# Kernel tuning notes

Hardware: AMD Instinct MI355X
Metric: run time of the kernel (lower is better)

Reference implementation:

```python
import jax, jax.numpy as jnp
import numpy as np

EPS = 1e-5

def yat_dense(x, kernel, bias, alpha):
    # scaled by (sqrt(F)/log(1+F))**alpha, plus bias.
    y = x @ kernel  # [..., F]
    dist = jnp.sum(x * x, axis=-1, keepdims=True) + jnp.sum(kernel * kernel, axis=0) - 2.0 * y
    out = (y * y) / (dist + EPS)
    F = kernel.shape[1]
    scale = (jnp.sqrt(jnp.float32(F)) / jnp.log1p(jnp.float32(F))) ** alpha
    return out * scale + bias

def setup_inputs() -> dict:
    key = jax.random.key(0)
    ks = jax.random.split(key, 8)
    B, T, C = 8, 1024, 1024
    x = jax.random.normal(ks[0], (B, T, C), dtype=jnp.float32)
    mask = jnp.tril(jnp.ones((T, T), dtype=bool))[None, None, :, :]  # causal [1,1,T,T]
    W_attn = jax.random.normal(ks[1], (C, 3 * C), dtype=jnp.float32) * (C ** -0.5)
    b_attn = jnp.zeros((3 * C,), dtype=jnp.float32)
    alpha_attn = jnp.ones((1,), dtype=jnp.float32)
    W_proj = jax.random.normal(ks[2], (C, C), dtype=jnp.float32) * (C ** -0.5)
    b_proj = jnp.zeros((C,), dtype=jnp.float32)
    alpha_proj = jnp.ones((1,), dtype=jnp.float32)
    return {"x": x, "mask": mask, "W_attn": W_attn, "b_attn": b_attn,
            "alpha_attn": alpha_attn, "W_proj": W_proj, "b_proj": b_proj,
            "alpha_proj": alpha_proj}

def reference(x, mask, W_attn, b_attn, alpha_attn, W_proj, b_proj, alpha_proj):
    B, T, C = x.shape
    H = 16
    hd = C // H
    qkv = yat_dense(x, W_attn, b_attn, alpha_attn)           # [B,T,3C]
    qkv = qkv.reshape(B, T, 3 * H, hd)
    q, k, v = jnp.array_split(qkv, 3, axis=2)                # each [B,T,H,hd]
    scale = 1.0 / jnp.sqrt(jnp.float32(hd))
    attn = jnp.einsum('bqhd,bkhd->bhqk', q, k) * scale       # [B,H,T,T]
    attn = jnp.where(mask, attn, jnp.finfo(jnp.float32).min)
    attn = jax.nn.softmax(attn, axis=-1)
    out = jnp.einsum('bhqk,bkhd->bqhd', attn, v).reshape(B, T, C)
    out = yat_dense(out, W_proj, b_proj, alpha_proj)         # [B,T,C]
    return out
```

## Files before the change

### kernel.cpp

```cpp
#include <hip/hip_runtime.h>
#include <math.h>

#define EPS 1e-5f
#define QSCALE 0.18033688011f

typedef short s16x8 __attribute__((ext_vector_type(8)));
typedef float f32x4 __attribute__((ext_vector_type(4)));
typedef unsigned short ushort_t;
typedef unsigned int uint_t;

__device__ inline ushort_t f2bf(float f) {
  uint_t u = __float_as_uint(f);
  uint_t r = (u + 0x7fffu + ((u >> 16) & 1u)) >> 16;
  return (ushort_t)r;
}
__device__ inline float bf2f(ushort_t h) {
  return __uint_as_float(((uint_t)h) << 16);
}
__device__ inline uint_t cvtpk_bf16(float lo, float hi) {
  uint_t r;
  asm("v_cvt_pk_bf16_f32 %0, %1, %2" : "=v"(r) : "v"(lo), "v"(hi));
  return r;
}

__global__ __launch_bounds__(256) void cast_k(const float* __restrict__ x,
                                              ushort_t* __restrict__ o, int n4) {
  const int i = (blockIdx.x * 256 + threadIdx.x);
  if (i >= n4) return;
  float4 v = *(const float4*)(x + (size_t)i * 4);
  *(ushort4*)(o + (size_t)i * 4) =
      make_ushort4(f2bf(v.x), f2bf(v.y), f2bf(v.z), f2bf(v.w));
}

__global__ __launch_bounds__(256) void transpose_cast_k(
    const float* __restrict__ W, ushort_t* __restrict__ o, int K, int N) {
  __shared__ float t[32][33];
  const int n0 = blockIdx.x * 32, k0 = blockIdx.y * 32;
  const int tx = threadIdx.x & 31, ty = threadIdx.x >> 5;
#pragma unroll
  for (int j = 0; j < 4; ++j)
    t[ty + j * 8][tx] = W[(size_t)(k0 + ty + j * 8) * N + n0 + tx];
  __syncthreads();
#pragma unroll
  for (int j = 0; j < 4; ++j)
    o[(size_t)(n0 + ty + j * 8) * K + k0 + tx] = f2bf(t[tx][ty + j * 8]);
}

__global__ __launch_bounds__(256) void rownorm_k(const float* __restrict__ X,
                                                 float* __restrict__ out, int K) {
  const int row = blockIdx.x * 4 + (threadIdx.x >> 6);
  const int lane = threadIdx.x & 63;
  const float4* p = (const float4*)(X + (size_t)row * K);
  float s = 0.f;
  const int nq = K >> 2;
  for (int i = lane; i < nq; i += 64) {
    float4 v = p[i];
    s += v.x * v.x + v.y * v.y + v.z * v.z + v.w * v.w;
  }
#pragma unroll
  for (int off = 1; off < 64; off <<= 1) s += __shfl_xor(s, off, 64);
  if (lane == 0) out[row] = s;
}

__global__ __launch_bounds__(256) void rownorm_bf16_k(const ushort_t* __restrict__ X,
                                                      float* __restrict__ out, int K) {
  const int row = blockIdx.x * 4 + (threadIdx.x >> 6);
  const int lane = threadIdx.x & 63;
  const ushort4* p = (const ushort4*)(X + (size_t)row * K);
  float s = 0.f;
  const int nq = K >> 2;
  for (int i = lane; i < nq; i += 64) {
    ushort4 v = p[i];
    float a = bf2f(v.x), b = bf2f(v.y), c = bf2f(v.z), d = bf2f(v.w);
    s += a * a + b * b + c * c + d * d;
  }
#pragma unroll
  for (int off = 1; off < 64; off <<= 1) s += __shfl_xor(s, off, 64);
  if (lane == 0) out[row] = s;
}

template <int MODE>
__global__ __launch_bounds__(256) void gemm_yat_mfma(
    const ushort_t* __restrict__ abf, const ushort_t* __restrict__ btbf,
    const float* __restrict__ bias, const float* __restrict__ alpha,
    const float* __restrict__ rown, const float* __restrict__ coln,
    void* __restrict__ outp, ushort_t* __restrict__ vtp, int M, int N, int K) {
  __shared__ alignas(16) short lds[2 * 8192];

  const int tid = threadIdx.x;
  const int wid = tid >> 6;
  const int lane = tid & 63;
  const int g = lane >> 4;
  const int wm = wid >> 1, wn = wid & 1;
  const int bm = blockIdx.y * 128;
  const int bn = blockIdx.x * 128;

  f32x4 acc[4][4];
#pragma unroll
  for (int m = 0; m < 4; ++m)
#pragma unroll
    for (int n = 0; n < 4; ++n) acc[m][n] = (f32x4){0.f, 0.f, 0.f, 0.f};

  const int kc_sw = ((lane & 3) - ((lane >> 3) & 3)) & 3;
  const int slot_rd = (g + ((lane & 15) >> 1)) & 3;

  auto stage = [&](int buf, int k0) {
#pragma unroll
    for (int j = 0; j < 4; ++j) {
      const int q = wid + 4 * j;
      const int reg_idx = q >> 3;
      const int i = q & 7;
      const int grow = i * 16 + (lane >> 2);
      const int gcol = k0 + kc_sw * 8;
      const ushort_t* src = (reg_idx == 0)
                                ? abf + (size_t)(bm + grow) * K + gcol
                                : btbf + (size_t)(bn + grow) * K + gcol;
      short* dst = &lds[buf * 8192 + reg_idx * 4096 + i * 512];
      __builtin_amdgcn_global_load_lds(
          (const __attribute__((address_space(1))) void*)src,
          (__attribute__((address_space(3))) void*)dst, 16, 0, 0);
    }
  };

  stage(0, 0);
  __syncthreads();

  int cur = 0;
  for (int k0 = 0; k0 < K; k0 += 32) {
    if (k0 + 32 < K) stage(cur ^ 1, k0 + 32);

    s16x8 af[4], bfr[4];
#pragma unroll
    for (int m = 0; m < 4; ++m) {
      const int off = cur * 8192 + (wm * 64 + m * 16 + (lane & 15)) * 32 + slot_rd * 8;
      af[m] = *(const s16x8*)&lds[off];
    }
#pragma unroll
    for (int n = 0; n < 4; ++n) {
      const int off = cur * 8192 + 4096 + (wn * 64 + n * 16 + (lane & 15)) * 32 + slot_rd * 8;
      bfr[n] = *(const s16x8*)&lds[off];
    }
    __builtin_amdgcn_s_setprio(1);
#pragma unroll
    for (int m = 0; m < 4; ++m)
#pragma unroll
      for (int n = 0; n < 4; ++n)
        acc[m][n] = __builtin_amdgcn_mfma_f32_16x16x32_bf16(af[m], bfr[n],
                                                            acc[m][n], 0, 0, 0);
    __builtin_amdgcn_s_setprio(0);
    __syncthreads();
    cur ^= 1;
  }

  const float sc = powf(sqrtf((float)N) / log1pf((float)N), alpha[0]);
  const int r0 = (lane >> 4) * 4;
  const int c0 = lane & 15;
#pragma unroll
  for (int m = 0; m < 4; ++m) {
    const int rowb = bm + wm * 64 + m * 16 + r0;
    float rn[4] = {rown[rowb], rown[rowb + 1], rown[rowb + 2], rown[rowb + 3]};
#pragma unroll
    for (int n = 0; n < 4; ++n) {
      const int col = bn + wn * 64 + n * 16 + c0;
      const float cn = coln[col];
      const float bs = bias[col];
      f32x4 a = acc[m][n];
      float o4[4];
#pragma unroll
      for (int r = 0; r < 4; ++r) {
        const float y = a[r];
        const float dist = rn[r] + cn - 2.f * y + EPS;
        o4[r] = (y * y) / dist * sc + bs;
      }
      if (MODE == 1) {
        if (col < 1024) {
#pragma unroll
          for (int r = 0; r < 4; ++r) o4[r] *= QSCALE;
        }
        if (col >= 2048) {
          const int d = col & 63, hh = (col >> 6) & 15;
          const int bb = rowb >> 10, t0 = rowb & 1023;
          ushort4 pk = make_ushort4(f2bf(o4[0]), f2bf(o4[1]), f2bf(o4[2]), f2bf(o4[3]));
          *(ushort4*)(vtp + (((size_t)(bb * 16 + hh) * 64 + d) << 10) + t0) = pk;
        } else {
#pragma unroll
          for (int r = 0; r < 4; ++r)
            ((ushort_t*)outp)[(size_t)(rowb + r) * N + col] = f2bf(o4[r]);
        }
      } else {
#pragma unroll
        for (int r = 0; r < 4; ++r)
          ((float*)outp)[(size_t)(rowb + r) * N + col] = o4[r];
      }
    }
  }
}

__global__ __launch_bounds__(256) void attn_mfma_k(const ushort_t* __restrict__ qkv,
                                                   const ushort_t* __restrict__ vt,
                                                   ushort_t* __restrict__ out) {
  const int i = blockIdx.y * 8 + blockIdx.x;
  const int xcd = i & 7, s = i >> 3;
  const int bh = xcd * 16 + (s & 15);
  const int pairx = s >> 4;
  const int b = bh >> 4, h = bh & 15;

  const int tid = threadIdx.x;
  const int wid = tid >> 6;
  const int lane = tid & 63;
  const int g = lane >> 4;
  const int c = lane & 15;

  __shared__ alignas(16) ushort_t Ks[64][76];
  __shared__ alignas(16) ushort_t Vs[64][76];
  __shared__ alignas(16) ushort_t Pl[4][16][76];

  const int srow = tid >> 3;
  const int sd0 = (tid & 7) * 8;
  const ushort_t* kbase = qkv + (size_t)(b * 1024) * 3072 + 1024 + h * 64;
  const ushort_t* vbase = vt + ((size_t)(b * 16 + h) << 16);

#pragma unroll
  for (int pass = 0; pass < 2; ++pass) {
    const int qt = pass == 0 ? pairx : 15 - pairx;

    const ushort_t* qrow =
        qkv + ((size_t)(b * 1024 + qt * 64 + wid * 16 + c)) * 3072 + h * 64;
    s16x8 qf[2];
    qf[0] = *(const s16x8*)(qrow + g * 8);
    qf[1] = *(const s16x8*)(qrow + 32 + g * 8);

    f32x4 acc_o[4];
#pragma unroll
    for (int dt = 0; dt < 4; ++dt) acc_o[dt] = (f32x4){0.f, 0.f, 0.f, 0.f};
    float m_loc = -INFINITY, l_loc = 0.f;

    for (int kt = 0; kt <= qt; ++kt) {
      s16x8 kreg[2], vreg[2];
#pragma unroll
      for (int ii = 0; ii < 2; ++ii) {
        kreg[ii] = *(const s16x8*)(kbase + (size_t)(kt * 64 + srow + ii * 32) * 3072 + sd0);
        vreg[ii] = *(const s16x8*)(vbase + (size_t)(srow + ii * 32) * 1024 + kt * 64 + sd0);
      }
      __syncthreads();
#pragma unroll
      for (int ii = 0; ii < 2; ++ii) {
        *(s16x8*)&Ks[srow + ii * 32][sd0] = kreg[ii];
        *(s16x8*)&Vs[srow + ii * 32][sd0] = vreg[ii];
      }
      __syncthreads();

      const bool diag = (kt == qt);
      const int jtmax = diag ? wid : 3;

      f32x4 sacc[4];
#pragma unroll
      for (int jt = 0; jt < 4; ++jt) sacc[jt] = (f32x4){0.f, 0.f, 0.f, 0.f};
      __builtin_amdgcn_s_setprio(1);
#pragma unroll
      for (int jt = 0; jt < 4; ++jt) {
        if (jt <= jtmax) {
          s16x8 kf0 = *(const s16x8*)&Ks[jt * 16 + c][g * 8];
          s16x8 kf1 = *(const s16x8*)&Ks[jt * 16 + c][32 + g * 8];
          sacc[jt] = __builtin_amdgcn_mfma_f32_16x16x32_bf16(kf0, qf[0], sacc[jt], 0, 0, 0);
          sacc[jt] = __builtin_amdgcn_mfma_f32_16x16x32_bf16(kf1, qf[1], sacc[jt], 0, 0, 0);
        }
      }
      __builtin_amdgcn_s_setprio(0);

      float sv[4][4];
#pragma unroll
      for (int jt = 0; jt < 4; ++jt)
#pragma unroll
        for (int r = 0; r < 4; ++r) {
          float v = sacc[jt][r];
          if (diag && (jt * 16 + g * 4 + r > wid * 16 + c)) v = -INFINITY;
          sv[jt][r] = v;
        }
      float mx = sv[0][0];
#pragma unroll
      for (int jt = 0; jt < 4; ++jt)
#pragma unroll
        for (int r = 0; r < 4; ++r) mx = fmaxf(mx, sv[jt][r]);
      mx = fmaxf(mx, __shfl_xor(mx, 16, 64));
      mx = fmaxf(mx, __shfl_xor(mx, 32, 64));
      const float mnew = fmaxf(m_loc, mx);
      const float al = exp2f(m_loc - mnew);
      m_loc = mnew;
      float p[4][4];
      float rs = 0.f;
#pragma unroll
      for (int jt = 0; jt < 4; ++jt)
#pragma unroll
        for (int r = 0; r < 4; ++r) {
          p[jt][r] = exp2f(sv[jt][r] - mnew);
          rs += p[jt][r];
        }
      rs += __shfl_xor(rs, 16, 64);
      rs += __shfl_xor(rs, 32, 64);
      l_loc = l_loc * al + rs;

      float al_bc[4];
#pragma unroll
      for (int r = 0; r < 4; ++r) al_bc[r] = __shfl(al, g * 4 + r, 16);
#pragma unroll
      for (int dt = 0; dt < 4; ++dt)
#pragma unroll
        for (int r = 0; r < 4; ++r) acc_o[dt][r] *= al_bc[r];

#pragma unroll
      for (int jt = 0; jt < 4; ++jt) {
        uint2 w;
        w.x = cvtpk_bf16(p[jt][0], p[jt][1]);
        w.y = cvtpk_bf16(p[jt][2], p[jt][3]);
        *(uint2*)&Pl[wid][c][jt * 16 + g * 4] = w;
      }

      const int kcmax = diag ? (wid >> 1) : 1;
      __builtin_amdgcn_s_setprio(1);
#pragma unroll
      for (int kc = 0; kc < 2; ++kc) {
        if (kc <= kcmax) {
          s16x8 pf = *(const s16x8*)&Pl[wid][c][kc * 32 + g * 8];
#pragma unroll
          for (int dt = 0; dt < 4; ++dt) {
            s16x8 vf = *(const s16x8*)&Vs[dt * 16 + c][kc * 32 + g * 8];
            acc_o[dt] = __builtin_amdgcn_mfma_f32_16x16x32_bf16(pf, vf, acc_o[dt], 0, 0, 0);
          }
        }
      }
      __builtin_amdgcn_s_setprio(0);
    }

    float l_bc[4];
#pragma unroll
    for (int r = 0; r < 4; ++r) l_bc[r] = __shfl(l_loc, g * 4 + r, 16);
#pragma unroll
    for (int r = 0; r < 4; ++r) {
      const float inv = 1.f / l_bc[r];
      ushort_t* op =
          out + ((size_t)(b * 1024 + qt * 64 + wid * 16 + g * 4 + r)) * 1024 + h * 64 + c;
#pragma unroll
      for (int dt = 0; dt < 4; ++dt) op[dt * 16] = f2bf(acc_o[dt][r] * inv);
    }
    __syncthreads();
  }
}

extern "C" void kernel_launch(void* const* d_in, const int* in_sizes, int n_in,
                              void* d_out, int out_size, void* d_ws, size_t ws_size,
                              hipStream_t stream) {
  const float* x = (const float*)d_in[0];
  const float* W_attn = (const float*)d_in[2];
  const float* b_attn = (const float*)d_in[3];
  const float* alpha_attn = (const float*)d_in[4];
  const float* W_proj = (const float*)d_in[5];
  const float* b_proj = (const float*)d_in[6];
  const float* alpha_proj = (const float*)d_in[7];
  float* out = (float*)d_out;

  char* ws = (char*)d_ws;
  ushort_t* qkv = (ushort_t*)(ws);
  ushort_t* attnout = (ushort_t*)(ws + 50331648ull);
  ushort_t* xbf = (ushort_t*)(ws + 67108864ull);
  ushort_t* watt = (ushort_t*)(ws + 83886080ull);
  ushort_t* wpjt = (ushort_t*)(ws + 90177536ull);
  float* xnorm = (float*)(ws + 92274688ull);
  float* anorm = (float*)(ws + 92307456ull);
  float* watn = (float*)(ws + 92340224ull);
  float* wpn = (float*)(ws + 92352512ull);
  ushort_t* vt = (ushort_t*)(ws + 92372992ull);

  const int M = 8192;

  cast_k<<<8192, 256, 0, stream>>>(x, xbf, M * 1024 / 4);
  transpose_cast_k<<<dim3(96, 32), 256, 0, stream>>>(W_attn, watt, 1024, 3072);
  transpose_cast_k<<<dim3(32, 32), 256, 0, stream>>>(W_proj, wpjt, 1024, 1024);
  rownorm_k<<<M / 4, 256, 0, stream>>>(x, xnorm, 1024);
  rownorm_bf16_k<<<3072 / 4, 256, 0, stream>>>(watt, watn, 1024);
  rownorm_bf16_k<<<1024 / 4, 256, 0, stream>>>(wpjt, wpn, 1024);

  gemm_yat_mfma<1><<<dim3(3072 / 128, M / 128), 256, 0, stream>>>(
      xbf, watt, b_attn, alpha_attn, xnorm, watn, (void*)qkv, vt, M, 3072, 1024);

  attn_mfma_k<<<dim3(8, 128), 256, 0, stream>>>(qkv, vt, attnout);

  rownorm_bf16_k<<<M / 4, 256, 0, stream>>>(attnout, anorm, 1024);

  gemm_yat_mfma<0><<<dim3(1024 / 128, M / 128), 256, 0, stream>>>(
      attnout, wpjt, b_proj, alpha_proj, anorm, wpn, (void*)out, nullptr, M, 1024, 1024);
}
```

Before: 189.4 us.

## Fuse cast with row norm, deepen GEMM K-tile, prefetch attention K/V tiles

```diff
diff --git a/kernel.cpp b/kernel.cpp
--- a/kernel.cpp
+++ b/kernel.cpp
@@ -23,13 +23,23 @@
   return r;
 }
 
-__global__ __launch_bounds__(256) void cast_k(const float* __restrict__ x,
-                                              ushort_t* __restrict__ o, int n4) {
-  const int i = (blockIdx.x * 256 + threadIdx.x);
-  if (i >= n4) return;
-  float4 v = *(const float4*)(x + (size_t)i * 4);
-  *(ushort4*)(o + (size_t)i * 4) =
-      make_ushort4(f2bf(v.x), f2bf(v.y), f2bf(v.z), f2bf(v.w));
+__global__ __launch_bounds__(256) void cast_norm_k(const float* __restrict__ x,
+                                                   ushort_t* __restrict__ xbf,
+                                                   float* __restrict__ xnorm) {
+  const int row = blockIdx.x * 4 + (threadIdx.x >> 6);
+  const int lane = threadIdx.x & 63;
+  const float4* p = (const float4*)(x + (size_t)row * 1024);
+  ushort4* o = (ushort4*)(xbf + (size_t)row * 1024);
+  float s = 0.f;
+#pragma unroll
+  for (int i = lane; i < 256; i += 64) {
+    float4 v = p[i];
+    s += v.x * v.x + v.y * v.y + v.z * v.z + v.w * v.w;
+    o[i] = make_ushort4(f2bf(v.x), f2bf(v.y), f2bf(v.z), f2bf(v.w));
+  }
+#pragma unroll
+  for (int off = 1; off < 64; off <<= 1) s += __shfl_xor(s, off, 64);
+  if (lane == 0) xnorm[row] = s;
 }
 
 __global__ __launch_bounds__(256) void transpose_cast_k(
@@ -44,22 +54,6 @@
 #pragma unroll
   for (int j = 0; j < 4; ++j)
     o[(size_t)(n0 + ty + j * 8) * K + k0 + tx] = f2bf(t[tx][ty + j * 8]);
-}
-
-__global__ __launch_bounds__(256) void rownorm_k(const float* __restrict__ X,
-                                                 float* __restrict__ out, int K) {
-  const int row = blockIdx.x * 4 + (threadIdx.x >> 6);
-  const int lane = threadIdx.x & 63;
-  const float4* p = (const float4*)(X + (size_t)row * K);
-  float s = 0.f;
-  const int nq = K >> 2;
-  for (int i = lane; i < nq; i += 64) {
-    float4 v = p[i];
-    s += v.x * v.x + v.y * v.y + v.z * v.z + v.w * v.w;
-  }
-#pragma unroll
-  for (int off = 1; off < 64; off <<= 1) s += __shfl_xor(s, off, 64);
-  if (lane == 0) out[row] = s;
 }
 
 __global__ __launch_bounds__(256) void rownorm_bf16_k(const ushort_t* __restrict__ X,
@@ -85,7 +79,7 @@
     const float* __restrict__ bias, const float* __restrict__ alpha,
     const float* __restrict__ rown, const float* __restrict__ coln,
     void* __restrict__ outp, ushort_t* __restrict__ vtp, int M, int N, int K) {
-  __shared__ alignas(16) short lds[2 * 8192];
+  __shared__ alignas(16) short lds[2 * 16384];
 
   const int tid = threadIdx.x;
   const int wid = tid >> 6;
@@ -106,16 +100,17 @@
 
   auto stage = [&](int buf, int k0) {
 #pragma unroll
-    for (int j = 0; j < 4; ++j) {
+    for (int j = 0; j < 8; ++j) {
       const int q = wid + 4 * j;
-      const int reg_idx = q >> 3;
-      const int i = q & 7;
-      const int grow = i * 16 + (lane >> 2);
-      const int gcol = k0 + kc_sw * 8;
+      const int reg_idx = q >> 4;
+      const int grp = (q >> 1) & 7;
+      const int half = q & 1;
+      const int grow = grp * 16 + (lane >> 2);
+      const int gcol = k0 + half * 32 + kc_sw * 8;
       const ushort_t* src = (reg_idx == 0)
                                 ? abf + (size_t)(bm + grow) * K + gcol
                                 : btbf + (size_t)(bn + grow) * K + gcol;
-      short* dst = &lds[buf * 8192 + reg_idx * 4096 + i * 512];
+      short* dst = &lds[buf * 16384 + reg_idx * 8192 + grp * 1024 + half * 512];
       __builtin_amdgcn_global_load_lds(
           (const __attribute__((address_space(1))) void*)src,
           (__attribute__((address_space(3))) void*)dst, 16, 0, 0);
@@ -126,27 +121,34 @@
   __syncthreads();
 
   int cur = 0;
-  for (int k0 = 0; k0 < K; k0 += 32) {
-    if (k0 + 32 < K) stage(cur ^ 1, k0 + 32);
-
-    s16x8 af[4], bfr[4];
-#pragma unroll
-    for (int m = 0; m < 4; ++m) {
-      const int off = cur * 8192 + (wm * 64 + m * 16 + (lane & 15)) * 32 + slot_rd * 8;
-      af[m] = *(const s16x8*)&lds[off];
-    }
-#pragma unroll
-    for (int n = 0; n < 4; ++n) {
-      const int off = cur * 8192 + 4096 + (wn * 64 + n * 16 + (lane & 15)) * 32 + slot_rd * 8;
-      bfr[n] = *(const s16x8*)&lds[off];
+  for (int k0 = 0; k0 < K; k0 += 64) {
+    if (k0 + 64 < K) stage(cur ^ 1, k0 + 64);
+
+    s16x8 af[2][4], bfr[2][4];
+#pragma unroll
+    for (int kk = 0; kk < 2; ++kk) {
+#pragma unroll
+      for (int m = 0; m < 4; ++m) {
+        const int off = cur * 16384 + (wm * 4 + m) * 1024 + kk * 512 +
+                        (lane & 15) * 32 + slot_rd * 8;
+        af[kk][m] = *(const s16x8*)&lds[off];
+      }
+#pragma unroll
+      for (int n = 0; n < 4; ++n) {
+        const int off = cur * 16384 + 8192 + (wn * 4 + n) * 1024 + kk * 512 +
+                        (lane & 15) * 32 + slot_rd * 8;
+        bfr[kk][n] = *(const s16x8*)&lds[off];
+      }
     }
     __builtin_amdgcn_s_setprio(1);
 #pragma unroll
-    for (int m = 0; m < 4; ++m)
-#pragma unroll
-      for (int n = 0; n < 4; ++n)
-        acc[m][n] = __builtin_amdgcn_mfma_f32_16x16x32_bf16(af[m], bfr[n],
-                                                            acc[m][n], 0, 0, 0);
+    for (int kk = 0; kk < 2; ++kk)
+#pragma unroll
+      for (int m = 0; m < 4; ++m)
+#pragma unroll
+        for (int n = 0; n < 4; ++n)
+          acc[m][n] = __builtin_amdgcn_mfma_f32_16x16x32_bf16(af[kk][m], bfr[kk][n],
+                                                              acc[m][n], 0, 0, 0);
     __builtin_amdgcn_s_setprio(0);
     __syncthreads();
     cur ^= 1;
@@ -235,13 +237,14 @@
     for (int dt = 0; dt < 4; ++dt) acc_o[dt] = (f32x4){0.f, 0.f, 0.f, 0.f};
     float m_loc = -INFINITY, l_loc = 0.f;
 
+    s16x8 kreg[2], vreg[2];
+#pragma unroll
+    for (int ii = 0; ii < 2; ++ii) {
+      kreg[ii] = *(const s16x8*)(kbase + (size_t)(srow + ii * 32) * 3072 + sd0);
+      vreg[ii] = *(const s16x8*)(vbase + (size_t)(srow + ii * 32) * 1024 + sd0);
+    }
+
     for (int kt = 0; kt <= qt; ++kt) {
-      s16x8 kreg[2], vreg[2];
-#pragma unroll
-      for (int ii = 0; ii < 2; ++ii) {
-        kreg[ii] = *(const s16x8*)(kbase + (size_t)(kt * 64 + srow + ii * 32) * 3072 + sd0);
-        vreg[ii] = *(const s16x8*)(vbase + (size_t)(srow + ii * 32) * 1024 + kt * 64 + sd0);
-      }
       __syncthreads();
 #pragma unroll
       for (int ii = 0; ii < 2; ++ii) {
@@ -249,6 +252,16 @@
         *(s16x8*)&Vs[srow + ii * 32][sd0] = vreg[ii];
       }
       __syncthreads();
+
+      if (kt < qt) {
+#pragma unroll
+        for (int ii = 0; ii < 2; ++ii) {
+          kreg[ii] = *(const s16x8*)(kbase +
+                                     (size_t)((kt + 1) * 64 + srow + ii * 32) * 3072 + sd0);
+          vreg[ii] = *(const s16x8*)(vbase + (size_t)(srow + ii * 32) * 1024 +
+                                     (kt + 1) * 64 + sd0);
+        }
+      }
 
       const bool diag = (kt == qt);
       const int jtmax = diag ? wid : 3;
@@ -343,7 +356,6 @@
 #pragma unroll
       for (int dt = 0; dt < 4; ++dt) op[dt * 16] = f2bf(acc_o[dt][r] * inv);
     }
-    __syncthreads();
   }
 }
 
@@ -373,10 +385,9 @@
 
   const int M = 8192;
 
-  cast_k<<<8192, 256, 0, stream>>>(x, xbf, M * 1024 / 4);
+  cast_norm_k<<<M / 4, 256, 0, stream>>>(x, xbf, xnorm);
   transpose_cast_k<<<dim3(96, 32), 256, 0, stream>>>(W_attn, watt, 1024, 3072);
   transpose_cast_k<<<dim3(32, 32), 256, 0, stream>>>(W_proj, wpjt, 1024, 1024);
-  rownorm_k<<<M / 4, 256, 0, stream>>>(x, xnorm, 1024);
   rownorm_bf16_k<<<3072 / 4, 256, 0, stream>>>(watt, watn, 1024);
   rownorm_bf16_k<<<1024 / 4, 256, 0, stream>>>(wpjt, wpn, 1024);
 
```

New measurement: 184.4 us. -2.6%, faster.
